# Kernel optimization log

Measured on AMD Instinct MI355X. Metric: run time of the kernel, lower is better.

Reference implementation:

```python
import jax, jax.numpy as jnp
import numpy as np

D = 256; H = 4; HD = 64; NL = 12; MAXP = 16; DIM = 8; PDIM = 4; B = 128
EPS = 1e-5
SCALE = float(np.sqrt(HD))


def _ln(x, g, b):
    m = jnp.mean(x, -1, keepdims=True)
    v = jnp.mean((x - m) ** 2, -1, keepdims=True)
    return (x - m) * jax.lax.rsqrt(v + EPS) * g + b


def _mha(xq, xkv, Wqkv, bqkv, Wo, bo, causal):
    # Wqkv is the packed PyTorch in_proj_weight [3D, D]
    Bq, S, _ = xq.shape
    K = xkv.shape[1]
    q = (xq @ Wqkv[:D].T + bqkv[:D]).reshape(Bq, S, H, HD).transpose(0, 2, 1, 3)
    k = (xkv @ Wqkv[D:2 * D].T + bqkv[D:2 * D]).reshape(Bq, K, H, HD).transpose(0, 2, 1, 3)
    v = (xkv @ Wqkv[2 * D:].T + bqkv[2 * D:]).reshape(Bq, K, H, HD).transpose(0, 2, 1, 3)
    s = jnp.einsum('bhqd,bhkd->bhqk', q, k) / SCALE
    if causal:
        s = jnp.where(jnp.tril(jnp.ones((S, K), bool)), s, -jnp.inf)
    a = jax.nn.softmax(s, -1)
    o = jnp.einsum('bhqk,bhkd->bhqd', a, v).transpose(0, 2, 1, 3).reshape(Bq, S, D)
    return o @ Wo.T + bo


def _decode(tgt, mem, p):
    # post-LN TransformerDecoder (norm_first=False), dropout in eval mode
    x = tgt
    for l in range(NL):
        x = _ln(x + _mha(x, x, p['sa_Wqkv'][l], p['sa_bqkv'][l], p['sa_Wo'][l], p['sa_bo'][l], True), p['ln1_g'][l], p['ln1_b'][l])
        x = _ln(x + _mha(x, mem, p['ca_Wqkv'][l], p['ca_bqkv'][l], p['ca_Wo'][l], p['ca_bo'][l], False), p['ln2_g'][l], p['ln2_b'][l])
        h = jax.nn.relu(x @ p['lin1_W'][l].T + p['lin1_b'][l])
        x = _ln(x + h @ p['lin2_W'][l].T + p['lin2_b'][l], p['ln3_g'][l], p['ln3_b'][l])
    return x


def _forward(U_real, U_imag, tok_W, tok_b, pos_emb, sa_Wqkv, sa_bqkv, sa_Wo, sa_bo, ca_Wqkv, ca_bqkv, ca_Wo, ca_bo, lin1_W, lin1_b, lin2_W, lin2_b, ln1_g, ln1_b, ln2_g, ln2_b, ln3_g, ln3_b, out_W, out_b, param_low, param_high):
    p = dict(sa_Wqkv=sa_Wqkv, sa_bqkv=sa_bqkv, sa_Wo=sa_Wo, sa_bo=sa_bo,
             ca_Wqkv=ca_Wqkv, ca_bqkv=ca_bqkv, ca_Wo=ca_Wo, ca_bo=ca_bo,
             lin1_W=lin1_W, lin1_b=lin1_b, lin2_W=lin2_W, lin2_b=lin2_b,
             ln1_g=ln1_g, ln1_b=ln1_b, ln2_g=ln2_g, ln2_b=ln2_b, ln3_g=ln3_g, ln3_b=ln3_b)
    Bq = U_real.shape[0]
    vec = jnp.concatenate([U_real.reshape(Bq, -1), U_imag.reshape(Bq, -1)], -1)  # [B, 2*dim^2]
    src = vec @ tok_W.T + tok_b  # [B, D]
    mem = src[:, None, :]  # [B, 1, D] cross-attn memory
    seq = [src]
    for i in range(MAXP):
        tgt = jnp.stack(seq, 1) + pos_emb[:i + 1][None]  # [B, i+1, D]
        x = _decode(tgt, mem, p)
        seq.append(x[:, -1])
    logits = jnp.stack(seq[1:], 1)  # [B, MAXP, D]
    pn = jax.nn.sigmoid(logits @ out_W.T + out_b)  # [B, MAXP, PDIM]
    return param_low + (param_high - param_low) * pn


def setup_inputs() -> dict:
    key = jax.random.key(0)
    ks = jax.random.split(key, 16)
    def w(k, shape, s=0.02):
        return jax.random.normal(k, shape, dtype=jnp.float32) * s
    return {
        'U_real': jax.random.normal(ks[0], (B, DIM, DIM), dtype=jnp.float32),
        'U_imag': jax.random.normal(ks[1], (B, DIM, DIM), dtype=jnp.float32),
        'tok_W': w(ks[2], (D, 2 * DIM * DIM)), 'tok_b': jnp.zeros((D,), jnp.float32),
        'pos_emb': w(ks[3], (MAXP + 1, D)),
        'sa_Wqkv': w(ks[4], (NL, 3 * D, D)), 'sa_bqkv': jnp.zeros((NL, 3 * D), jnp.float32),
        'sa_Wo': w(ks[5], (NL, D, D)), 'sa_bo': jnp.zeros((NL, D), jnp.float32),
        'ca_Wqkv': w(ks[6], (NL, 3 * D, D)), 'ca_bqkv': jnp.zeros((NL, 3 * D), jnp.float32),
        'ca_Wo': w(ks[7], (NL, D, D)), 'ca_bo': jnp.zeros((NL, D), jnp.float32),
        'lin1_W': w(ks[8], (NL, 4 * D, D)), 'lin1_b': jnp.zeros((NL, 4 * D), jnp.float32),
        'lin2_W': w(ks[9], (NL, D, 4 * D)), 'lin2_b': jnp.zeros((NL, D), jnp.float32),
        'ln1_g': jnp.ones((NL, D), jnp.float32), 'ln1_b': jnp.zeros((NL, D), jnp.float32),
        'ln2_g': jnp.ones((NL, D), jnp.float32), 'ln2_b': jnp.zeros((NL, D), jnp.float32),
        'ln3_g': jnp.ones((NL, D), jnp.float32), 'ln3_b': jnp.zeros((NL, D), jnp.float32),
        'out_W': w(ks[10], (PDIM, D)), 'out_b': jnp.zeros((PDIM,), jnp.float32),
        'param_low': jnp.array([-1.0, 0.0, 0.0, 0.0], jnp.float32),
        'param_high': jnp.array([1.0, 1.0, 6.2832, 1.0], jnp.float32),
    }


def reference(U_real, U_imag, tok_W, tok_b, pos_emb, sa_Wqkv, sa_bqkv, sa_Wo, sa_bo, ca_Wqkv, ca_bqkv, ca_Wo, ca_bo, lin1_W, lin1_b, lin2_W, lin2_b, ln1_g, ln1_b, ln2_g, ln2_b, ln3_g, ln3_b, out_W, out_b, param_low, param_high):
    return _forward(U_real, U_imag, tok_W, tok_b, pos_emb, sa_Wqkv, sa_bqkv, sa_Wo, sa_bo, ca_Wqkv, ca_bqkv, ca_Wo, ca_bo, lin1_W, lin1_b, lin2_W, lin2_b, ln1_g, ln1_b, ln2_g, ln2_b, ln3_g, ln3_b, out_W, out_b, param_low, param_high)
```

## Files before the change

kernel.cpp:

```cpp
#include <hip/hip_runtime.h>
#include <hip/hip_bf16.h>


typedef __attribute__((ext_vector_type(8))) short short8;
typedef __attribute__((ext_vector_type(4))) float f32x4;

#define EPS_ 1e-5f

__device__ __forceinline__ unsigned short f2b(float x){
  union { float f; unsigned u; } c; c.f = x;
  unsigned r = (c.u + 0x7fffu + ((c.u >> 16) & 1u)) >> 16;
  return (unsigned short)r;
}
__device__ __forceinline__ float b2f(unsigned short u){
  union { unsigned u; float f; } c; c.u = ((unsigned)u) << 16;
  return c.f;
}
__device__ __forceinline__ unsigned long long pack4b(const f32x4 a){
  return (unsigned long long)f2b(a[0]) |
         ((unsigned long long)f2b(a[1]) << 16) |
         ((unsigned long long)f2b(a[2]) << 32) |
         ((unsigned long long)f2b(a[3]) << 48);
}
__device__ __forceinline__ unsigned long long pack2f(float a, float b){
  union { float f; unsigned u; } x, y; x.f = a; y.f = b;
  return (unsigned long long)x.u | ((unsigned long long)y.u << 32);
}
__device__ __forceinline__ float lo_f(unsigned long long v){
  union { unsigned u; float f; } c; c.u = (unsigned)v; return c.f;
}
__device__ __forceinline__ float hi_f(unsigned long long v){
  union { unsigned u; float f; } c; c.u = (unsigned)(v >> 32); return c.f;
}

#define AL(p)    __hip_atomic_load((p),  __ATOMIC_RELAXED, __HIP_MEMORY_SCOPE_AGENT)
#define AS(p,v)  __hip_atomic_store((p), (v), __ATOMIC_RELAXED, __HIP_MEMORY_SCOPE_AGENT)

#define OFF_WQKV 0ull
#define OFF_WO   4718592ull
#define OFF_L1   6291456ull
#define OFF_L2   12582912ull
#define OFF_SRC  18874368ull
#define OFF_CC   19005440ull
#define OFF_KV   19791872ull
#define OFF_XH   44957696ull
#define OFF_ZA   45219840ull
#define OFF_ZB   45613056ull
#define OFF_FLG  46006272ull

__global__ void k_conv(const float* __restrict__ wqkv, const float* __restrict__ wo,
                       const float* __restrict__ l1, const float* __restrict__ l2,
                       unsigned short* __restrict__ dst){
  const long long n0 = 12LL*768*256;
  const long long n1 = n0 + 12LL*256*256;
  const long long n2 = n1 + 12LL*1024*256;
  const long long n3 = n2 + 12LL*256*1024;
  for (long long idx = (long long)blockIdx.x*256 + threadIdx.x; idx < n3;
       idx += (long long)gridDim.x*256){
    float v;
    if (idx < n0) v = wqkv[idx];
    else if (idx < n1) v = wo[idx - n0];
    else if (idx < n2) v = l1[idx - n1];
    else v = l2[idx - n2];
    dst[idx] = f2b(v);
  }
}

__global__ void k_src(const float* __restrict__ U_real, const float* __restrict__ U_imag,
                      const float* __restrict__ tok_W, const float* __restrict__ tok_b,
                      const float* __restrict__ pos,
                      float* __restrict__ src, float* __restrict__ xh0){
  int b = blockIdx.x, n = threadIdx.x;
  const float* w = tok_W + n*128;
  const float* ur = U_real + b*64;
  const float* ui = U_imag + b*64;
  float acc = tok_b[n];
  #pragma unroll 8
  for (int k = 0; k < 64; ++k) acc += w[k]*ur[k];
  #pragma unroll 8
  for (int k = 0; k < 64; ++k) acc += w[64+k]*ui[k];
  src[b*256+n] = acc;
  xh0[b*256+n] = acc + pos[n];
}

__global__ void k_cc(const float* __restrict__ caW, const float* __restrict__ cab,
                     const float* __restrict__ caWo, const float* __restrict__ cabo,
                     const float* __restrict__ src, unsigned short* __restrict__ cc){
  int l = blockIdx.x >> 7, b = blockIdx.x & 127, t = threadIdx.x;
  __shared__ float v[256];
  const float* s = src + b*256;
  {
    const float* w = caW + ((long long)l*768 + 512 + t)*256;
    float a = cab[l*768 + 512 + t];
    #pragma unroll 8
    for (int k = 0; k < 256; ++k) a += w[k]*s[k];
    v[t] = a;
  }
  __syncthreads();
  {
    const float* w = caWo + ((long long)l*256 + t)*256;
    float a = cabo[l*256 + t];
    #pragma unroll 8
    for (int k = 0; k < 256; ++k) a += w[k]*v[k];
    cc[((long long)l*128 + b)*256 + t] = f2b(a);
  }
}

#define PUBW(FARR) do{                                                       \
  __syncthreads();                                                           \
  if (tid == 0) AS(FARR + l*4 + h, seq);                                     \
  if (tid < 3){                                                              \
    int ho = tid + (tid >= h ? 1 : 0);                                       \
    const int* fp = FARR + l*4 + ho;                                         \
    while (AL(fp) < seq) __builtin_amdgcn_s_sleep(2);                        \
  }                                                                          \
  __syncthreads();                                                           \
}while(0)

__global__ __launch_bounds__(512, 1) void k_main(
  const unsigned short* __restrict__ wqkv,
  const unsigned short* __restrict__ wo,
  const unsigned short* __restrict__ wl1,
  const unsigned short* __restrict__ wl2,
  const float* __restrict__ bqkv, const float* __restrict__ bo_,
  const float* __restrict__ bl1,  const float* __restrict__ bl2,
  const float* __restrict__ g1, const float* __restrict__ be1,
  const float* __restrict__ g2, const float* __restrict__ be2,
  const float* __restrict__ g3, const float* __restrict__ be3,
  const unsigned short* __restrict__ cc,
  const float* __restrict__ pos,
  const float* __restrict__ outW,
  const float* __restrict__ outb,
  const float* __restrict__ plow, const float* __restrict__ phigh,
  unsigned short* __restrict__ kvc,
  unsigned long long* __restrict__ xh,
  unsigned long long* __restrict__ zA,
  unsigned long long* __restrict__ zB,
  int* __restrict__ flags,
  float* __restrict__ out)
{
  __shared__ float xf[16][260];
  __shared__ float zf[16][260];
  __shared__ float yf[16][260];
  __shared__ unsigned short xb[16][264];
  __shared__ unsigned short hs[16][264];
  __shared__ unsigned short qs[16][72];
  __shared__ unsigned short os[16][72];

  const int tid  = threadIdx.x;
  const int w    = tid >> 6, lane = tid & 63;
  const int l    = blockIdx.x >> 2;
  const int h    = blockIdx.x & 3;
  const int mrow = lane & 15, kgrp = lane >> 4;

  int* fin = flags;
  int* fA  = flags + 384;
  int* fB  = flags + 432;

  for (int t = 0; t < 16; ++t){
    for (int g = 0; g < 8; ++g){
      const int seq = t*8 + g + 1;

      {
        int need = (l == 0) ? t : (t+1);
        if (need > 0 && tid < 4){
          const int* fp = fin + (l*4 + tid)*8 + g;
          while (AL(fp) < need) __builtin_amdgcn_s_sleep(2);
        }
        __syncthreads();
        int row = tid >> 5, c8 = (tid & 31)*8;
        const unsigned long long* xp =
            xh + (((size_t)(l & 1)*8 + g)*16 + row)*128 + (c8 >> 1);
        #pragma unroll
        for (int j = 0; j < 4; ++j){
          unsigned long long v = AL(xp + j);
          float f0 = lo_f(v), f1 = hi_f(v);
          xf[row][c8+2*j]   = f0;  xf[row][c8+2*j+1] = f1;
          xb[row][c8+2*j]   = f2b(f0);
          xb[row][c8+2*j+1] = f2b(f1);
        }
      }
      __syncthreads();

      {
        short8 a[8];
        #pragma unroll
        for (int kc = 0; kc < 8; ++kc)
          a[kc] = *(const short8*)&xb[mrow][kc*32 + kgrp*8];
        const unsigned short* wl = wqkv + (size_t)l*196608;
        for (int t2 = w; t2 < 12; t2 += 8){
          int p = t2 >> 2, q4 = t2 & 3;
          int n_l = q4*16 + mrow;
          const unsigned short* wp = wl + (size_t)(p*256 + h*64 + n_l)*256 + kgrp*8;
          f32x4 acc = {0,0,0,0};
          #pragma unroll
          for (int kc = 0; kc < 8; ++kc){
            short8 b0 = *(const short8*)(wp + kc*32);
            acc = __builtin_amdgcn_mfma_f32_16x16x32_bf16(a[kc], b0, acc, 0,0,0);
          }
          float bias = bqkv[l*768 + p*256 + h*64 + n_l];
          #pragma unroll
          for (int r = 0; r < 4; ++r){
            int br = kgrp*4 + r;
            float v = acc[r] + bias;
            if (p == 0){
              qs[br][n_l] = f2b(v);
            } else {
              size_t kb = (((((size_t)l*4 + h)*8 + g)*16 + br)*16 + t)*128
                          + (p == 2 ? 64 : 0) + n_l;
              kvc[kb] = f2b(v);
            }
          }
        }
      }
      __syncthreads();

      {
        int row = w*2 + (lane >> 5);
        int lid = lane & 31;
        float q0 = b2f(qs[row][lid*2]), q1 = b2f(qs[row][lid*2+1]);
        const unsigned short* base =
            kvc + (((((size_t)l*4 + h)*8 + g)*16 + row)*16)*128 + lid*2;
        float sv[16];
        #pragma unroll
        for (int j = 0; j < 16; ++j){
          if (j <= t){
            const unsigned short* kp = base + j*128;
            float p = q0*b2f(kp[0]) + q1*b2f(kp[1]);
            p += __shfl_xor(p, 1);
            p += __shfl_xor(p, 2);
            p += __shfl_xor(p, 4);
            p += __shfl_xor(p, 8);
            p += __shfl_xor(p, 16);
            sv[j] = p * 0.125f;
          } else sv[j] = -1e30f;
        }
        float mx = sv[0];
        #pragma unroll
        for (int j = 1; j < 16; ++j) mx = fmaxf(mx, sv[j]);
        float den = 0.f, e[16];
        #pragma unroll
        for (int j = 0; j < 16; ++j){ e[j] = __expf(sv[j]-mx); den += e[j]; }
        float rd = 1.f/den;
        float o0 = 0.f, o1 = 0.f;
        #pragma unroll
        for (int j = 0; j < 16; ++j){
          if (j <= t){
            const unsigned short* vp = base + j*128 + 64;
            o0 += e[j]*b2f(vp[0]);
            o1 += e[j]*b2f(vp[1]);
          }
        }
        os[row][lid*2]   = f2b(o0*rd);
        os[row][lid*2+1] = f2b(o1*rd);
      }
      __syncthreads();

      {
        short8 a2[2];
        #pragma unroll
        for (int kc = 0; kc < 2; ++kc)
          a2[kc] = *(const short8*)&os[mrow][kc*32 + kgrp*8];
        #pragma unroll
        for (int u2 = 0; u2 < 2; ++u2){
          int n_g = (w*2+u2)*16 + mrow;
          const unsigned short* wp = wo + (size_t)l*65536 + (size_t)n_g*256 + h*64 + kgrp*8;
          f32x4 acc = {0,0,0,0};
          #pragma unroll
          for (int kc = 0; kc < 2; ++kc){
            short8 b0 = *(const short8*)(wp + kc*32);
            acc = __builtin_amdgcn_mfma_f32_16x16x32_bf16(a2[kc], b0, acc, 0,0,0);
          }
          AS(zA + ((size_t)(l*4 + h)*256 + n_g)*4 + kgrp, pack4b(acc));
        }
      }
      PUBW(fA);

      {
        int col = tid & 255, rq2 = tid >> 8;
        float a8[8] = {0,0,0,0,0,0,0,0};
        #pragma unroll
        for (int s4 = 0; s4 < 4; ++s4){
          const unsigned long long* bp = zA + ((size_t)(l*4 + s4)*256 + col)*4 + rq2*2;
          #pragma unroll
          for (int q = 0; q < 2; ++q){
            unsigned long long v = AL(bp + q);
            a8[q*4+0] += b2f((unsigned short)v);
            a8[q*4+1] += b2f((unsigned short)(v >> 16));
            a8[q*4+2] += b2f((unsigned short)(v >> 32));
            a8[q*4+3] += b2f((unsigned short)(v >> 48));
          }
        }
        float bias = bo_[l*256 + col];
        #pragma unroll
        for (int r = 0; r < 8; ++r){
          int row = rq2*8 + r;
          zf[row][col] = a8[r] + bias + xf[row][col];
        }
      }
      __syncthreads();

      {
        int row = tid >> 5, c8 = (tid & 31)*8;
        float tt[8];
        #pragma unroll
        for (int k = 0; k < 8; ++k) tt[k] = zf[row][c8+k];
        float sm = 0, sq = 0;
        #pragma unroll
        for (int k = 0; k < 8; ++k){ sm += tt[k]; sq += tt[k]*tt[k]; }
        sm += __shfl_xor(sm,1);  sq += __shfl_xor(sq,1);
        sm += __shfl_xor(sm,2);  sq += __shfl_xor(sq,2);
        sm += __shfl_xor(sm,4);  sq += __shfl_xor(sq,4);
        sm += __shfl_xor(sm,8);  sq += __shfl_xor(sq,8);
        sm += __shfl_xor(sm,16); sq += __shfl_xor(sq,16);
        float mean = sm*(1.f/256), var = sq*(1.f/256) - mean*mean;
        float rs = rsqrtf(var + EPS_);
        const float* g1p = g1 + l*256 + c8;
        const float* b1p = be1 + l*256 + c8;
        const unsigned short* ccp = cc + ((size_t)l*128 + g*16 + row)*256 + c8;
        #pragma unroll
        for (int k = 0; k < 8; ++k)
          tt[k] = (tt[k]-mean)*rs*g1p[k] + b1p[k] + b2f(ccp[k]);
        sm = 0; sq = 0;
        #pragma unroll
        for (int k = 0; k < 8; ++k){ sm += tt[k]; sq += tt[k]*tt[k]; }
        sm += __shfl_xor(sm,1);  sq += __shfl_xor(sq,1);
        sm += __shfl_xor(sm,2);  sq += __shfl_xor(sq,2);
        sm += __shfl_xor(sm,4);  sq += __shfl_xor(sq,4);
        sm += __shfl_xor(sm,8);  sq += __shfl_xor(sq,8);
        sm += __shfl_xor(sm,16); sq += __shfl_xor(sq,16);
        mean = sm*(1.f/256); var = sq*(1.f/256) - mean*mean;
        rs = rsqrtf(var + EPS_);
        const float* g2p = g2 + l*256 + c8;
        const float* b2p = be2 + l*256 + c8;
        #pragma unroll
        for (int k = 0; k < 8; ++k){
          float y = (tt[k]-mean)*rs*g2p[k] + b2p[k];
          yf[row][c8+k] = y;
          xb[row][c8+k] = f2b(y);
        }
      }
      __syncthreads();

      {
        short8 a[8];
        #pragma unroll
        for (int kc = 0; kc < 8; ++kc)
          a[kc] = *(const short8*)&xb[mrow][kc*32 + kgrp*8];
        const unsigned short* wl = wl1 + (size_t)l*262144;
        #pragma unroll
        for (int u2 = 0; u2 < 2; ++u2){
          int n_sl = (w*2+u2)*16 + mrow;
          const unsigned short* wp = wl + (size_t)(h*256 + n_sl)*256 + kgrp*8;
          f32x4 acc = {0,0,0,0};
          #pragma unroll
          for (int kc = 0; kc < 8; ++kc){
            short8 b0 = *(const short8*)(wp + kc*32);
            acc = __builtin_amdgcn_mfma_f32_16x16x32_bf16(a[kc], b0, acc, 0,0,0);
          }
          float bias = bl1[l*1024 + h*256 + n_sl];
          #pragma unroll
          for (int r = 0; r < 4; ++r){
            float hv = acc[r] + bias;
            hs[kgrp*4 + r][n_sl] = f2b(hv > 0.f ? hv : 0.f);
          }
        }
      }
      __syncthreads();

      {
        short8 ah[8];
        #pragma unroll
        for (int kc = 0; kc < 8; ++kc)
          ah[kc] = *(const short8*)&hs[mrow][kc*32 + kgrp*8];
        #pragma unroll
        for (int u2 = 0; u2 < 2; ++u2){
          int n_g = (w*2+u2)*16 + mrow;
          const unsigned short* wp = wl2 + (size_t)l*262144 + (size_t)n_g*1024 + h*256 + kgrp*8;
          f32x4 acc = {0,0,0,0};
          #pragma unroll
          for (int kc = 0; kc < 8; ++kc){
            short8 b0 = *(const short8*)(wp + kc*32);
            acc = __builtin_amdgcn_mfma_f32_16x16x32_bf16(ah[kc], b0, acc, 0,0,0);
          }
          AS(zB + ((size_t)(l*4 + h)*256 + n_g)*4 + kgrp, pack4b(acc));
        }
      }
      PUBW(fB);

      {
        int col = tid & 255, rq2 = tid >> 8;
        float a8[8] = {0,0,0,0,0,0,0,0};
        #pragma unroll
        for (int s4 = 0; s4 < 4; ++s4){
          const unsigned long long* bp = zB + ((size_t)(l*4 + s4)*256 + col)*4 + rq2*2;
          #pragma unroll
          for (int q = 0; q < 2; ++q){
            unsigned long long v = AL(bp + q);
            a8[q*4+0] += b2f((unsigned short)v);
            a8[q*4+1] += b2f((unsigned short)(v >> 16));
            a8[q*4+2] += b2f((unsigned short)(v >> 32));
            a8[q*4+3] += b2f((unsigned short)(v >> 48));
          }
        }
        float bias = bl2[l*256 + col];
        #pragma unroll
        for (int r = 0; r < 8; ++r){
          int row = rq2*8 + r;
          zf[row][col] = a8[r] + bias + yf[row][col];
        }
      }
      __syncthreads();

      {
        int row = tid >> 5, c8 = (tid & 31)*8;
        float tt[8];
        #pragma unroll
        for (int k = 0; k < 8; ++k) tt[k] = zf[row][c8+k];
        float sm = 0, sq = 0;
        #pragma unroll
        for (int k = 0; k < 8; ++k){ sm += tt[k]; sq += tt[k]*tt[k]; }
        sm += __shfl_xor(sm,1);  sq += __shfl_xor(sq,1);
        sm += __shfl_xor(sm,2);  sq += __shfl_xor(sq,2);
        sm += __shfl_xor(sm,4);  sq += __shfl_xor(sq,4);
        sm += __shfl_xor(sm,8);  sq += __shfl_xor(sq,8);
        sm += __shfl_xor(sm,16); sq += __shfl_xor(sq,16);
        float mean = sm*(1.f/256), var = sq*(1.f/256) - mean*mean;
        float rs = rsqrtf(var + EPS_);
        const float* g3p = g3 + l*256 + c8;
        const float* b3p = be3 + l*256 + c8;
        float xn[8];
        #pragma unroll
        for (int k = 0; k < 8; ++k)
          xn[k] = (tt[k]-mean)*rs*g3p[k] + b3p[k];
        if (l == 11){
          if (h == 0){
            float pr[4];
            #pragma unroll
            for (int p = 0; p < 4; ++p){
              float a = 0.f;
              #pragma unroll
              for (int k = 0; k < 8; ++k) a += xn[k]*outW[p*256 + c8 + k];
              a += __shfl_xor(a,1); a += __shfl_xor(a,2);
              a += __shfl_xor(a,4); a += __shfl_xor(a,8);
              a += __shfl_xor(a,16);
              pr[p] = a;
            }
            if ((tid & 31) == 0){
              int gr = g*16 + row;
              #pragma unroll
              for (int p = 0; p < 4; ++p){
                float v2 = pr[p] + outb[p];
                float sg = 1.f/(1.f + __expf(-v2));
                out[((size_t)gr*16 + t)*4 + p] = plow[p] + (phigh[p]-plow[p])*sg;
              }
            }
          }
          if (t < 15){
            const float* pp = pos + (t+1)*256 + c8;
            #pragma unroll
            for (int k = 0; k < 8; ++k) xn[k] += pp[k];
          }
        }
        bool last = (l == 11) && (t == 15);
        if (!last && ((c8 >> 6) == h)){
          unsigned long long* xp =
              xh + (((size_t)((l+1) & 1)*8 + g)*16 + row)*128 + (c8 >> 1);
          #pragma unroll
          for (int j = 0; j < 4; ++j)
            AS(xp + j, pack2f(xn[2*j], xn[2*j+1]));
        }
      }
      __syncthreads();
      if (!((l == 11) && (t == 15)) && tid == 0)
        AS(fin + ((((l+1) % 12)*4) + h)*8 + g, t+1);
    }
  }
}

extern "C" void kernel_launch(void* const* d_in, const int* in_sizes, int n_in,
                              void* d_out, int out_size, void* d_ws, size_t ws_size,
                              hipStream_t stream) {
  const float* U_real = (const float*)d_in[0];
  const float* U_imag = (const float*)d_in[1];
  const float* tok_W  = (const float*)d_in[2];
  const float* tok_b  = (const float*)d_in[3];
  const float* pos    = (const float*)d_in[4];
  const float* saW    = (const float*)d_in[5];
  const float* sab    = (const float*)d_in[6];
  const float* saWo   = (const float*)d_in[7];
  const float* sabo   = (const float*)d_in[8];
  const float* caW    = (const float*)d_in[9];
  const float* cab    = (const float*)d_in[10];
  const float* caWo   = (const float*)d_in[11];
  const float* cabo   = (const float*)d_in[12];
  const float* l1W    = (const float*)d_in[13];
  const float* l1b    = (const float*)d_in[14];
  const float* l2W    = (const float*)d_in[15];
  const float* l2b    = (const float*)d_in[16];
  const float* g1     = (const float*)d_in[17];
  const float* be1    = (const float*)d_in[18];
  const float* g2     = (const float*)d_in[19];
  const float* be2    = (const float*)d_in[20];
  const float* g3     = (const float*)d_in[21];
  const float* be3    = (const float*)d_in[22];
  const float* outW   = (const float*)d_in[23];
  const float* outb   = (const float*)d_in[24];
  const float* plow   = (const float*)d_in[25];
  const float* phigh  = (const float*)d_in[26];

  char* ws = (char*)d_ws;
  unsigned short* wb        = (unsigned short*)(ws + OFF_WQKV);
  float* srcb               = (float*)(ws + OFF_SRC);
  unsigned short* ccb       = (unsigned short*)(ws + OFF_CC);
  unsigned short* kvc       = (unsigned short*)(ws + OFF_KV);
  unsigned long long* xhb   = (unsigned long long*)(ws + OFF_XH);
  unsigned long long* zAb   = (unsigned long long*)(ws + OFF_ZA);
  unsigned long long* zBb   = (unsigned long long*)(ws + OFF_ZB);
  int* flags                = (int*)(ws + OFF_FLG);

  (void)hipMemsetAsync(ws + OFF_FLG, 0, 4096, stream);
  k_conv<<<dim3(4608), dim3(256), 0, stream>>>(saW, saWo, l1W, l2W, wb);
  k_src<<<dim3(128), dim3(256), 0, stream>>>(U_real, U_imag, tok_W, tok_b, pos,
                                             srcb, (float*)xhb);
  k_cc<<<dim3(1536), dim3(256), 0, stream>>>(caW, cab, caWo, cabo, srcb, ccb);
  k_main<<<dim3(48), dim3(512), 0, stream>>>(
      wb,
      (unsigned short*)(ws + OFF_WO),
      (unsigned short*)(ws + OFF_L1),
      (unsigned short*)(ws + OFF_L2),
      sab, sabo, l1b, l2b,
      g1, be1, g2, be2, g3, be3,
      ccb, pos, outW, outb, plow, phigh,
      kvc, xhb, zAb, zBb, flags, (float*)d_out);
}
```

Baseline: 4.761 ms.

## Split batch groups across more persistent blocks with XCD-aware mapping

The persistent pipelined kernel grows from 48 to 48*GS blocks (GS up to 4, chosen from workspace size), each handling a subset of the 8 batch groups for its layer/head. Block indices are remapped so that the four head blocks of a layer share an XCD, and the split-K scratch and flag arrays are sized per sub-group. The layer-done flag is now published before the output head writes, and spin sleep is shortened. This aims to use more CUs and shorten the serial chain, but adds more flag polling traffic and more weight reads from cache.

```diff
diff --git a/kernel.cpp b/kernel.cpp
--- a/kernel.cpp
+++ b/kernel.cpp
@@ -44,9 +44,7 @@
 #define OFF_CC   19005440ull
 #define OFF_KV   19791872ull
 #define OFF_XH   44957696ull
-#define OFF_ZA   45219840ull
-#define OFF_ZB   45613056ull
-#define OFF_FLG  46006272ull
+#define OFF_DYN  45219840ull
 
 __global__ void k_conv(const float* __restrict__ wqkv, const float* __restrict__ wo,
                        const float* __restrict__ l1, const float* __restrict__ l2,
@@ -108,11 +106,11 @@
 
 #define PUBW(FARR) do{                                                       \
   __syncthreads();                                                           \
-  if (tid == 0) AS(FARR + l*4 + h, seq);                                     \
+  if (tid == 0) AS(FARR + quad*4 + h, seq);                                  \
   if (tid < 3){                                                              \
     int ho = tid + (tid >= h ? 1 : 0);                                       \
-    const int* fp = FARR + l*4 + ho;                                         \
-    while (AL(fp) < seq) __builtin_amdgcn_s_sleep(2);                        \
+    const int* fp = FARR + quad*4 + ho;                                      \
+    while (AL(fp) < seq) __builtin_amdgcn_s_sleep(1);                        \
   }                                                                          \
   __syncthreads();                                                           \
 }while(0)
@@ -137,6 +135,7 @@
   unsigned long long* __restrict__ zA,
   unsigned long long* __restrict__ zB,
   int* __restrict__ flags,
+  int GS, int lgGS,
   float* __restrict__ out)
 {
   __shared__ float xf[16][260];
@@ -149,35 +148,45 @@
 
   const int tid  = threadIdx.x;
   const int w    = tid >> 6, lane = tid & 63;
-  const int l    = blockIdx.x >> 2;
-  const int h    = blockIdx.x & 3;
   const int mrow = lane & 15, kgrp = lane >> 4;
+
+  const int xcd      = blockIdx.x & 7;
+  const int q        = blockIdx.x >> 3;
+  const int j        = q & (GS - 1);
+  const int pairSlot = q >> lgGS;
+  const int pair     = xcd + 8*pairSlot;
+  const int l        = pair >> 2;
+  const int h        = pair & 3;
+  const int quad     = l*GS + j;
+  const int GPB      = 8 >> lgGS;
+  const int g0       = j*GPB;
 
   int* fin = flags;
   int* fA  = flags + 384;
-  int* fB  = flags + 432;
+  int* fB  = fA + 48*GS;
 
   for (int t = 0; t < 16; ++t){
-    for (int g = 0; g < 8; ++g){
-      const int seq = t*8 + g + 1;
+    for (int gg = 0; gg < GPB; ++gg){
+      const int g   = g0 + gg;
+      const int seq = t*GPB + gg + 1;
 
       {
         int need = (l == 0) ? t : (t+1);
         if (need > 0 && tid < 4){
           const int* fp = fin + (l*4 + tid)*8 + g;
-          while (AL(fp) < need) __builtin_amdgcn_s_sleep(2);
+          while (AL(fp) < need) __builtin_amdgcn_s_sleep(1);
         }
         __syncthreads();
         int row = tid >> 5, c8 = (tid & 31)*8;
         const unsigned long long* xp =
-            xh + (((size_t)(l & 1)*8 + g)*16 + row)*128 + (c8 >> 1);
-        #pragma unroll
-        for (int j = 0; j < 4; ++j){
-          unsigned long long v = AL(xp + j);
+            xh + ((size_t)(l & 1)*8 + g)*2048 + (size_t)row*128 + (c8 >> 1);
+        #pragma unroll
+        for (int jj = 0; jj < 4; ++jj){
+          unsigned long long v = AL(xp + jj);
           float f0 = lo_f(v), f1 = hi_f(v);
-          xf[row][c8+2*j]   = f0;  xf[row][c8+2*j+1] = f1;
-          xb[row][c8+2*j]   = f2b(f0);
-          xb[row][c8+2*j+1] = f2b(f1);
+          xf[row][c8+2*jj]   = f0;  xf[row][c8+2*jj+1] = f1;
+          xb[row][c8+2*jj]   = f2b(f0);
+          xb[row][c8+2*jj+1] = f2b(f1);
         }
       }
       __syncthreads();
@@ -218,37 +227,37 @@
       {
         int row = w*2 + (lane >> 5);
         int lid = lane & 31;
-        float q0 = b2f(qs[row][lid*2]), q1 = b2f(qs[row][lid*2+1]);
+        float q0v = b2f(qs[row][lid*2]), q1v = b2f(qs[row][lid*2+1]);
         const unsigned short* base =
             kvc + (((((size_t)l*4 + h)*8 + g)*16 + row)*16)*128 + lid*2;
         float sv[16];
         #pragma unroll
-        for (int j = 0; j < 16; ++j){
-          if (j <= t){
-            const unsigned short* kp = base + j*128;
-            float p = q0*b2f(kp[0]) + q1*b2f(kp[1]);
+        for (int jj = 0; jj < 16; ++jj){
+          if (jj <= t){
+            const unsigned short* kp = base + jj*128;
+            float p = q0v*b2f(kp[0]) + q1v*b2f(kp[1]);
             p += __shfl_xor(p, 1);
             p += __shfl_xor(p, 2);
             p += __shfl_xor(p, 4);
             p += __shfl_xor(p, 8);
             p += __shfl_xor(p, 16);
-            sv[j] = p * 0.125f;
-          } else sv[j] = -1e30f;
+            sv[jj] = p * 0.125f;
+          } else sv[jj] = -1e30f;
         }
         float mx = sv[0];
         #pragma unroll
-        for (int j = 1; j < 16; ++j) mx = fmaxf(mx, sv[j]);
+        for (int jj = 1; jj < 16; ++jj) mx = fmaxf(mx, sv[jj]);
         float den = 0.f, e[16];
         #pragma unroll
-        for (int j = 0; j < 16; ++j){ e[j] = __expf(sv[j]-mx); den += e[j]; }
+        for (int jj = 0; jj < 16; ++jj){ e[jj] = __expf(sv[jj]-mx); den += e[jj]; }
         float rd = 1.f/den;
         float o0 = 0.f, o1 = 0.f;
         #pragma unroll
-        for (int j = 0; j < 16; ++j){
-          if (j <= t){
-            const unsigned short* vp = base + j*128 + 64;
-            o0 += e[j]*b2f(vp[0]);
-            o1 += e[j]*b2f(vp[1]);
+        for (int jj = 0; jj < 16; ++jj){
+          if (jj <= t){
+            const unsigned short* vp = base + jj*128 + 64;
+            o0 += e[jj]*b2f(vp[0]);
+            o1 += e[jj]*b2f(vp[1]);
           }
         }
         os[row][lid*2]   = f2b(o0*rd);
@@ -271,7 +280,7 @@
             short8 b0 = *(const short8*)(wp + kc*32);
             acc = __builtin_amdgcn_mfma_f32_16x16x32_bf16(a2[kc], b0, acc, 0,0,0);
           }
-          AS(zA + ((size_t)(l*4 + h)*256 + n_g)*4 + kgrp, pack4b(acc));
+          AS(zA + ((size_t)(quad*4 + h)*256 + n_g)*4 + kgrp, pack4b(acc));
         }
       }
       PUBW(fA);
@@ -281,14 +290,14 @@
         float a8[8] = {0,0,0,0,0,0,0,0};
         #pragma unroll
         for (int s4 = 0; s4 < 4; ++s4){
-          const unsigned long long* bp = zA + ((size_t)(l*4 + s4)*256 + col)*4 + rq2*2;
-          #pragma unroll
-          for (int q = 0; q < 2; ++q){
-            unsigned long long v = AL(bp + q);
-            a8[q*4+0] += b2f((unsigned short)v);
-            a8[q*4+1] += b2f((unsigned short)(v >> 16));
-            a8[q*4+2] += b2f((unsigned short)(v >> 32));
-            a8[q*4+3] += b2f((unsigned short)(v >> 48));
+          const unsigned long long* bp = zA + ((size_t)(quad*4 + s4)*256 + col)*4 + rq2*2;
+          #pragma unroll
+          for (int qq = 0; qq < 2; ++qq){
+            unsigned long long v = AL(bp + qq);
+            a8[qq*4+0] += b2f((unsigned short)v);
+            a8[qq*4+1] += b2f((unsigned short)(v >> 16));
+            a8[qq*4+2] += b2f((unsigned short)(v >> 32));
+            a8[qq*4+3] += b2f((unsigned short)(v >> 48));
           }
         }
         float bias = bo_[l*256 + col];
@@ -383,7 +392,7 @@
             short8 b0 = *(const short8*)(wp + kc*32);
             acc = __builtin_amdgcn_mfma_f32_16x16x32_bf16(ah[kc], b0, acc, 0,0,0);
           }
-          AS(zB + ((size_t)(l*4 + h)*256 + n_g)*4 + kgrp, pack4b(acc));
+          AS(zB + ((size_t)(quad*4 + h)*256 + n_g)*4 + kgrp, pack4b(acc));
         }
       }
       PUBW(fB);
@@ -393,14 +402,14 @@
         float a8[8] = {0,0,0,0,0,0,0,0};
         #pragma unroll
         for (int s4 = 0; s4 < 4; ++s4){
-          const unsigned long long* bp = zB + ((size_t)(l*4 + s4)*256 + col)*4 + rq2*2;
-          #pragma unroll
-          for (int q = 0; q < 2; ++q){
-            unsigned long long v = AL(bp + q);
-            a8[q*4+0] += b2f((unsigned short)v);
-            a8[q*4+1] += b2f((unsigned short)(v >> 16));
-            a8[q*4+2] += b2f((unsigned short)(v >> 32));
-            a8[q*4+3] += b2f((unsigned short)(v >> 48));
+          const unsigned long long* bp = zB + ((size_t)(quad*4 + s4)*256 + col)*4 + rq2*2;
+          #pragma unroll
+          for (int qq = 0; qq < 2; ++qq){
+            unsigned long long v = AL(bp + qq);
+            a8[qq*4+0] += b2f((unsigned short)v);
+            a8[qq*4+1] += b2f((unsigned short)(v >> 16));
+            a8[qq*4+2] += b2f((unsigned short)(v >> 32));
+            a8[qq*4+3] += b2f((unsigned short)(v >> 48));
           }
         }
         float bias = bl2[l*256 + col];
@@ -433,47 +442,47 @@
         #pragma unroll
         for (int k = 0; k < 8; ++k)
           xn[k] = (tt[k]-mean)*rs*g3p[k] + b3p[k];
-        if (l == 11){
-          if (h == 0){
-            float pr[4];
+
+        float pr[4] = {0,0,0,0};
+        const bool doHead = (l == 11) && (h == 0);
+        if (doHead){
+          #pragma unroll
+          for (int p = 0; p < 4; ++p){
+            float a = 0.f;
             #pragma unroll
-            for (int p = 0; p < 4; ++p){
-              float a = 0.f;
-              #pragma unroll
-              for (int k = 0; k < 8; ++k) a += xn[k]*outW[p*256 + c8 + k];
-              a += __shfl_xor(a,1); a += __shfl_xor(a,2);
-              a += __shfl_xor(a,4); a += __shfl_xor(a,8);
-              a += __shfl_xor(a,16);
-              pr[p] = a;
-            }
-            if ((tid & 31) == 0){
-              int gr = g*16 + row;
-              #pragma unroll
-              for (int p = 0; p < 4; ++p){
-                float v2 = pr[p] + outb[p];
-                float sg = 1.f/(1.f + __expf(-v2));
-                out[((size_t)gr*16 + t)*4 + p] = plow[p] + (phigh[p]-plow[p])*sg;
-              }
-            }
-          }
-          if (t < 15){
-            const float* pp = pos + (t+1)*256 + c8;
-            #pragma unroll
-            for (int k = 0; k < 8; ++k) xn[k] += pp[k];
-          }
-        }
-        bool last = (l == 11) && (t == 15);
+            for (int k = 0; k < 8; ++k) a += xn[k]*outW[p*256 + c8 + k];
+            a += __shfl_xor(a,1); a += __shfl_xor(a,2);
+            a += __shfl_xor(a,4); a += __shfl_xor(a,8);
+            a += __shfl_xor(a,16);
+            pr[p] = a;
+          }
+        }
+        if (l == 11 && t < 15){
+          const float* pp = pos + (t+1)*256 + c8;
+          #pragma unroll
+          for (int k = 0; k < 8; ++k) xn[k] += pp[k];
+        }
+        const bool last = (l == 11) && (t == 15);
         if (!last && ((c8 >> 6) == h)){
           unsigned long long* xp =
-              xh + (((size_t)((l+1) & 1)*8 + g)*16 + row)*128 + (c8 >> 1);
-          #pragma unroll
-          for (int j = 0; j < 4; ++j)
-            AS(xp + j, pack2f(xn[2*j], xn[2*j+1]));
-        }
-      }
-      __syncthreads();
-      if (!((l == 11) && (t == 15)) && tid == 0)
-        AS(fin + ((((l+1) % 12)*4) + h)*8 + g, t+1);
+              xh + ((size_t)((l+1) & 1)*8 + g)*2048 + (size_t)row*128 + (c8 >> 1);
+          #pragma unroll
+          for (int jj = 0; jj < 4; ++jj)
+            AS(xp + jj, pack2f(xn[2*jj], xn[2*jj+1]));
+        }
+        __syncthreads();
+        if (!last && tid == 0)
+          AS(fin + (((l+1) % 12)*4 + h)*8 + g, t+1);
+        if (doHead && ((tid & 31) == 0)){
+          int gr = g*16 + row;
+          #pragma unroll
+          for (int p = 0; p < 4; ++p){
+            float v2 = pr[p] + outb[p];
+            float sg = 1.f/(1.f + __expf(-v2));
+            out[((size_t)gr*16 + t)*4 + p] = plow[p] + (phigh[p]-plow[p])*sg;
+          }
+        }
+      }
     }
   }
 }
@@ -509,22 +518,33 @@
   const float* plow   = (const float*)d_in[25];
   const float* phigh  = (const float*)d_in[26];
 
+  int GS = 1, lgGS = 0;
+  {
+    auto need = [](int gs) -> size_t {
+      size_t za = (size_t)12 * gs * 4 * 256 * 4 * 8;
+      return (size_t)OFF_DYN + 2*za + 4096;
+    };
+    if (ws_size >= need(4))      { GS = 4; lgGS = 2; }
+    else if (ws_size >= need(2)) { GS = 2; lgGS = 1; }
+  }
+  size_t zaBytes = (size_t)12 * GS * 4 * 256 * 4 * 8;
+
   char* ws = (char*)d_ws;
   unsigned short* wb        = (unsigned short*)(ws + OFF_WQKV);
   float* srcb               = (float*)(ws + OFF_SRC);
   unsigned short* ccb       = (unsigned short*)(ws + OFF_CC);
   unsigned short* kvc       = (unsigned short*)(ws + OFF_KV);
   unsigned long long* xhb   = (unsigned long long*)(ws + OFF_XH);
-  unsigned long long* zAb   = (unsigned long long*)(ws + OFF_ZA);
-  unsigned long long* zBb   = (unsigned long long*)(ws + OFF_ZB);
-  int* flags                = (int*)(ws + OFF_FLG);
-
-  (void)hipMemsetAsync(ws + OFF_FLG, 0, 4096, stream);
+  unsigned long long* zAb   = (unsigned long long*)(ws + OFF_DYN);
+  unsigned long long* zBb   = (unsigned long long*)(ws + OFF_DYN + zaBytes);
+  int* flags                = (int*)(ws + OFF_DYN + 2*zaBytes);
+
+  (void)hipMemsetAsync(ws + OFF_DYN + 2*zaBytes, 0, 4096, stream);
   k_conv<<<dim3(4608), dim3(256), 0, stream>>>(saW, saWo, l1W, l2W, wb);
   k_src<<<dim3(128), dim3(256), 0, stream>>>(U_real, U_imag, tok_W, tok_b, pos,
                                              srcb, (float*)xhb);
   k_cc<<<dim3(1536), dim3(256), 0, stream>>>(caW, cab, caWo, cabo, srcb, ccb);
-  k_main<<<dim3(48), dim3(512), 0, stream>>>(
+  k_main<<<dim3(48*GS), dim3(512), 0, stream>>>(
       wb,
       (unsigned short*)(ws + OFF_WO),
       (unsigned short*)(ws + OFF_L1),
@@ -532,5 +552,5 @@
       sab, sabo, l1b, l2b,
       g1, be1, g2, be2, g3, be3,
       ccb, pos, outW, outb, plow, phigh,
-      kvc, xhb, zAb, zBb, flags, (float*)d_out);
-}
+      kvc, xhb, zAb, zBb, flags, GS, lgGS, (float*)d_out);
+}
```

New measurement: 5.063 ms. 1.06x slower.

## Pre-swizzle bf16 weights into MFMA tile order and stage via global_load_lds

Applied to the files above, without the earlier changes.

The conversion kernel now writes each weight matrix in a per-layer, per-head, per-16-column-tile layout that matches the MFMA B-operand lane order. The main kernel loads each tile with contiguous 16-byte global-to-LDS loads into a per-wave staging buffer, replacing strided global reads. It also shortens the spin-wait sleep and publishes the next-layer flag before writing the output head so downstream blocks start earlier. The cost is 64KB of extra LDS for staging and a full vmcnt wait before each tile's MFMAs, which serialises load and compute within a wave.

```diff
diff --git a/kernel.cpp b/kernel.cpp
--- a/kernel.cpp
+++ b/kernel.cpp
@@ -35,6 +35,15 @@
 
 #define AL(p)    __hip_atomic_load((p),  __ATOMIC_RELAXED, __HIP_MEMORY_SCOPE_AGENT)
 #define AS(p,v)  __hip_atomic_store((p), (v), __ATOMIC_RELAXED, __HIP_MEMORY_SCOPE_AGENT)
+
+__device__ __forceinline__ void gload16(const unsigned short* g, unsigned short* l){
+  __builtin_amdgcn_global_load_lds(
+      (const __attribute__((address_space(1))) unsigned int*)g,
+      (__attribute__((address_space(3))) unsigned int*)l, 16, 0, 0);
+}
+#define WAIT_STG() do{ asm volatile("s_waitcnt vmcnt(0)" ::: "memory");      \
+                       __builtin_amdgcn_sched_barrier(0); }while(0)
+#define PIN_ORDER() __builtin_amdgcn_sched_barrier(0)
 
 #define OFF_WQKV 0ull
 #define OFF_WO   4718592ull
@@ -51,17 +60,49 @@
 __global__ void k_conv(const float* __restrict__ wqkv, const float* __restrict__ wo,
                        const float* __restrict__ l1, const float* __restrict__ l2,
                        unsigned short* __restrict__ dst){
-  const long long n0 = 12LL*768*256;
-  const long long n1 = n0 + 12LL*256*256;
-  const long long n2 = n1 + 12LL*1024*256;
-  const long long n3 = n2 + 12LL*256*1024;
-  for (long long idx = (long long)blockIdx.x*256 + threadIdx.x; idx < n3;
+  const long long nQ = 2359296, nW = 786432, nL1 = 3145728;
+  const long long tot = 9437184;
+  for (long long idx = (long long)blockIdx.x*256 + threadIdx.x; idx < tot;
        idx += (long long)gridDim.x*256){
     float v;
-    if (idx < n0) v = wqkv[idx];
-    else if (idx < n1) v = wo[idx - n0];
-    else if (idx < n2) v = l1[idx - n1];
-    else v = l2[idx - n2];
+    long long i = idx;
+    if (i < nQ){
+      int l = (int)(i/196608); int r = (int)(i%196608);
+      int h = r/49152; r %= 49152;
+      int tile = r/4096; r %= 4096;
+      int kc = r>>9; int lane = (r>>3)&63; int e = r&7;
+      int p = tile>>2, q4 = tile&3;
+      int n = p*256 + h*64 + q4*16 + (lane&15);
+      int k = (lane>>4)*8 + kc*32 + e;
+      v = wqkv[((long long)l*768 + n)*256 + k];
+    } else if (i < nQ+nW){
+      i -= nQ;
+      int l = (int)(i/65536); int r = (int)(i%65536);
+      int h = r/16384; r %= 16384;
+      int tile = r/1024; r %= 1024;
+      int kc = r>>9; int lane = (r>>3)&63; int e = r&7;
+      int n = tile*16 + (lane&15);
+      int k = h*64 + (lane>>4)*8 + kc*32 + e;
+      v = wo[((long long)l*256 + n)*256 + k];
+    } else if (i < nQ+nW+nL1){
+      i -= nQ+nW;
+      int l = (int)(i/262144); int r = (int)(i%262144);
+      int h = r/65536; r %= 65536;
+      int tile = r/4096; r %= 4096;
+      int kc = r>>9; int lane = (r>>3)&63; int e = r&7;
+      int n = h*256 + tile*16 + (lane&15);
+      int k = (lane>>4)*8 + kc*32 + e;
+      v = l1[((long long)l*1024 + n)*256 + k];
+    } else {
+      i -= nQ+nW+nL1;
+      int l = (int)(i/262144); int r = (int)(i%262144);
+      int h = r/65536; r %= 65536;
+      int tile = r/4096; r %= 4096;
+      int kc = r>>9; int lane = (r>>3)&63; int e = r&7;
+      int n = tile*16 + (lane&15);
+      int k = h*256 + (lane>>4)*8 + kc*32 + e;
+      v = l2[((long long)l*256 + n)*1024 + k];
+    }
     dst[idx] = f2b(v);
   }
 }
@@ -112,7 +153,7 @@
   if (tid < 3){                                                              \
     int ho = tid + (tid >= h ? 1 : 0);                                       \
     const int* fp = FARR + l*4 + ho;                                         \
-    while (AL(fp) < seq) __builtin_amdgcn_s_sleep(2);                        \
+    while (AL(fp) < seq) __builtin_amdgcn_s_sleep(1);                        \
   }                                                                          \
   __syncthreads();                                                           \
 }while(0)
@@ -146,6 +187,7 @@
   __shared__ unsigned short hs[16][264];
   __shared__ unsigned short qs[16][72];
   __shared__ unsigned short os[16][72];
+  __shared__ __align__(16) unsigned short stg[8][4096];
 
   const int tid  = threadIdx.x;
   const int w    = tid >> 6, lane = tid & 63;
@@ -157,6 +199,12 @@
   int* fA  = flags + 384;
   int* fB  = flags + 432;
 
+  const unsigned short* pQ  = wqkv + (size_t)(l*4 + h)*12*4096;
+  const unsigned short* pWo = wo   + (size_t)(l*4 + h)*16*1024;
+  const unsigned short* pL1 = wl1  + (size_t)(l*4 + h)*16*4096;
+  const unsigned short* pL2 = wl2  + (size_t)(l*4 + h)*16*4096;
+  unsigned short* sb = &stg[w][0];
+
   for (int t = 0; t < 16; ++t){
     for (int g = 0; g < 8; ++g){
       const int seq = t*8 + g + 1;
@@ -165,12 +213,12 @@
         int need = (l == 0) ? t : (t+1);
         if (need > 0 && tid < 4){
           const int* fp = fin + (l*4 + tid)*8 + g;
-          while (AL(fp) < need) __builtin_amdgcn_s_sleep(2);
+          while (AL(fp) < need) __builtin_amdgcn_s_sleep(1);
         }
         __syncthreads();
         int row = tid >> 5, c8 = (tid & 31)*8;
         const unsigned long long* xp =
-            xh + (((size_t)(l & 1)*8 + g)*16 + row)*128 + (c8 >> 1);
+            xh + ((size_t)(l & 1)*8 + g)*2048 + (size_t)row*128 + (c8 >> 1);
         #pragma unroll
         for (int j = 0; j < 4; ++j){
           unsigned long long v = AL(xp + j);
@@ -187,17 +235,22 @@
         #pragma unroll
         for (int kc = 0; kc < 8; ++kc)
           a[kc] = *(const short8*)&xb[mrow][kc*32 + kgrp*8];
-        const unsigned short* wl = wqkv + (size_t)l*196608;
-        for (int t2 = w; t2 < 12; t2 += 8){
-          int p = t2 >> 2, q4 = t2 & 3;
+        int nt = (w < 4) ? 2 : 1;
+        for (int it = 0; it < nt; ++it){
+          int tile = (it == 0) ? w : (8 + w);
+          const unsigned short* src = pQ + (size_t)tile*4096;
+          #pragma unroll
+          for (int j = 0; j < 8; ++j)
+            gload16(src + j*512 + lane*8, sb + j*512);
+          WAIT_STG();
+          f32x4 acc = {0,0,0,0};
+          #pragma unroll
+          for (int kc = 0; kc < 8; ++kc){
+            short8 b0 = *(const short8*)(sb + kc*512 + lane*8);
+            acc = __builtin_amdgcn_mfma_f32_16x16x32_bf16(a[kc], b0, acc, 0,0,0);
+          }
+          int p = tile >> 2, q4 = tile & 3;
           int n_l = q4*16 + mrow;
-          const unsigned short* wp = wl + (size_t)(p*256 + h*64 + n_l)*256 + kgrp*8;
-          f32x4 acc = {0,0,0,0};
-          #pragma unroll
-          for (int kc = 0; kc < 8; ++kc){
-            short8 b0 = *(const short8*)(wp + kc*32);
-            acc = __builtin_amdgcn_mfma_f32_16x16x32_bf16(a[kc], b0, acc, 0,0,0);
-          }
           float bias = bqkv[l*768 + p*256 + h*64 + n_l];
           #pragma unroll
           for (int r = 0; r < 4; ++r){
@@ -211,6 +264,7 @@
               kvc[kb] = f2b(v);
             }
           }
+          PIN_ORDER();
         }
       }
       __syncthreads();
@@ -261,18 +315,23 @@
         #pragma unroll
         for (int kc = 0; kc < 2; ++kc)
           a2[kc] = *(const short8*)&os[mrow][kc*32 + kgrp*8];
+        const unsigned short* src = pWo + (size_t)(w*2)*1024;
+        #pragma unroll
+        for (int j = 0; j < 4; ++j)
+          gload16(src + j*512 + lane*8, sb + j*512);
+        WAIT_STG();
         #pragma unroll
         for (int u2 = 0; u2 < 2; ++u2){
           int n_g = (w*2+u2)*16 + mrow;
-          const unsigned short* wp = wo + (size_t)l*65536 + (size_t)n_g*256 + h*64 + kgrp*8;
           f32x4 acc = {0,0,0,0};
           #pragma unroll
           for (int kc = 0; kc < 2; ++kc){
-            short8 b0 = *(const short8*)(wp + kc*32);
+            short8 b0 = *(const short8*)(sb + u2*1024 + kc*512 + lane*8);
             acc = __builtin_amdgcn_mfma_f32_16x16x32_bf16(a2[kc], b0, acc, 0,0,0);
           }
           AS(zA + ((size_t)(l*4 + h)*256 + n_g)*4 + kgrp, pack4b(acc));
         }
+        PIN_ORDER();
       }
       PUBW(fA);
 
@@ -347,23 +406,27 @@
         #pragma unroll
         for (int kc = 0; kc < 8; ++kc)
           a[kc] = *(const short8*)&xb[mrow][kc*32 + kgrp*8];
-        const unsigned short* wl = wl1 + (size_t)l*262144;
-        #pragma unroll
-        for (int u2 = 0; u2 < 2; ++u2){
-          int n_sl = (w*2+u2)*16 + mrow;
-          const unsigned short* wp = wl + (size_t)(h*256 + n_sl)*256 + kgrp*8;
+        for (int it = 0; it < 2; ++it){
+          int tile = w*2 + it;
+          const unsigned short* src = pL1 + (size_t)tile*4096;
+          #pragma unroll
+          for (int j = 0; j < 8; ++j)
+            gload16(src + j*512 + lane*8, sb + j*512);
+          WAIT_STG();
           f32x4 acc = {0,0,0,0};
           #pragma unroll
           for (int kc = 0; kc < 8; ++kc){
-            short8 b0 = *(const short8*)(wp + kc*32);
+            short8 b0 = *(const short8*)(sb + kc*512 + lane*8);
             acc = __builtin_amdgcn_mfma_f32_16x16x32_bf16(a[kc], b0, acc, 0,0,0);
           }
+          int n_sl = tile*16 + mrow;
           float bias = bl1[l*1024 + h*256 + n_sl];
           #pragma unroll
           for (int r = 0; r < 4; ++r){
             float hv = acc[r] + bias;
             hs[kgrp*4 + r][n_sl] = f2b(hv > 0.f ? hv : 0.f);
           }
+          PIN_ORDER();
         }
       }
       __syncthreads();
@@ -373,17 +436,22 @@
         #pragma unroll
         for (int kc = 0; kc < 8; ++kc)
           ah[kc] = *(const short8*)&hs[mrow][kc*32 + kgrp*8];
-        #pragma unroll
-        for (int u2 = 0; u2 < 2; ++u2){
-          int n_g = (w*2+u2)*16 + mrow;
-          const unsigned short* wp = wl2 + (size_t)l*262144 + (size_t)n_g*1024 + h*256 + kgrp*8;
+        for (int it = 0; it < 2; ++it){
+          int tile = w*2 + it;
+          const unsigned short* src = pL2 + (size_t)tile*4096;
+          #pragma unroll
+          for (int j = 0; j < 8; ++j)
+            gload16(src + j*512 + lane*8, sb + j*512);
+          WAIT_STG();
           f32x4 acc = {0,0,0,0};
           #pragma unroll
           for (int kc = 0; kc < 8; ++kc){
-            short8 b0 = *(const short8*)(wp + kc*32);
+            short8 b0 = *(const short8*)(sb + kc*512 + lane*8);
             acc = __builtin_amdgcn_mfma_f32_16x16x32_bf16(ah[kc], b0, acc, 0,0,0);
           }
+          int n_g = tile*16 + mrow;
           AS(zB + ((size_t)(l*4 + h)*256 + n_g)*4 + kgrp, pack4b(acc));
+          PIN_ORDER();
         }
       }
       PUBW(fB);
@@ -433,47 +501,47 @@
         #pragma unroll
         for (int k = 0; k < 8; ++k)
           xn[k] = (tt[k]-mean)*rs*g3p[k] + b3p[k];
-        if (l == 11){
-          if (h == 0){
-            float pr[4];
+
+        float pr[4] = {0,0,0,0};
+        const bool doHead = (l == 11) && (h == 0);
+        if (doHead){
+          #pragma unroll
+          for (int p = 0; p < 4; ++p){
+            float a = 0.f;
             #pragma unroll
-            for (int p = 0; p < 4; ++p){
-              float a = 0.f;
-              #pragma unroll
-              for (int k = 0; k < 8; ++k) a += xn[k]*outW[p*256 + c8 + k];
-              a += __shfl_xor(a,1); a += __shfl_xor(a,2);
-              a += __shfl_xor(a,4); a += __shfl_xor(a,8);
-              a += __shfl_xor(a,16);
-              pr[p] = a;
-            }
-            if ((tid & 31) == 0){
-              int gr = g*16 + row;
-              #pragma unroll
-              for (int p = 0; p < 4; ++p){
-                float v2 = pr[p] + outb[p];
-                float sg = 1.f/(1.f + __expf(-v2));
-                out[((size_t)gr*16 + t)*4 + p] = plow[p] + (phigh[p]-plow[p])*sg;
-              }
-            }
-          }
-          if (t < 15){
-            const float* pp = pos + (t+1)*256 + c8;
-            #pragma unroll
-            for (int k = 0; k < 8; ++k) xn[k] += pp[k];
-          }
-        }
-        bool last = (l == 11) && (t == 15);
+            for (int k = 0; k < 8; ++k) a += xn[k]*outW[p*256 + c8 + k];
+            a += __shfl_xor(a,1); a += __shfl_xor(a,2);
+            a += __shfl_xor(a,4); a += __shfl_xor(a,8);
+            a += __shfl_xor(a,16);
+            pr[p] = a;
+          }
+        }
+        if (l == 11 && t < 15){
+          const float* pp = pos + (t+1)*256 + c8;
+          #pragma unroll
+          for (int k = 0; k < 8; ++k) xn[k] += pp[k];
+        }
+        const bool last = (l == 11) && (t == 15);
         if (!last && ((c8 >> 6) == h)){
           unsigned long long* xp =
-              xh + (((size_t)((l+1) & 1)*8 + g)*16 + row)*128 + (c8 >> 1);
+              xh + ((size_t)((l+1) & 1)*8 + g)*2048 + (size_t)row*128 + (c8 >> 1);
           #pragma unroll
           for (int j = 0; j < 4; ++j)
             AS(xp + j, pack2f(xn[2*j], xn[2*j+1]));
         }
-      }
-      __syncthreads();
-      if (!((l == 11) && (t == 15)) && tid == 0)
-        AS(fin + ((((l+1) % 12)*4) + h)*8 + g, t+1);
+        __syncthreads();
+        if (!last && tid == 0)
+          AS(fin + (((l+1) % 12)*4 + h)*8 + g, t+1);
+        if (doHead && ((tid & 31) == 0)){
+          int gr = g*16 + row;
+          #pragma unroll
+          for (int p = 0; p < 4; ++p){
+            float v2 = pr[p] + outb[p];
+            float sg = 1.f/(1.f + __expf(-v2));
+            out[((size_t)gr*16 + t)*4 + p] = plow[p] + (phigh[p]-plow[p])*sg;
+          }
+        }
+      }
     }
   }
 }
```

Result: faster. 4.527 ms, median of 2 (-4.9%).
